# Performance work log

Measured on AMD Instinct MI355X. Metric: run time of the kernel, lower is better.

Reference implementation:

```python
import jax, jax.numpy as jnp
import numpy as np

N, F_IN, HID, OUT, H = 10000, 256, 256, 512, 4
E = 320000
SLOPE = 0.2  # GATv2Conv default negative_slope
EPS = 1e-5   # LayerNorm eps


def setup_inputs() -> dict:
    key = jax.random.key(0)
    ks = jax.random.split(key, 10)
    g = lambda k, shape, fan: (jax.random.normal(k, shape, jnp.float32) / np.float32(np.sqrt(fan)))
    d1, d2 = HID // H, OUT // H
    return {
        "x": jax.random.normal(ks[0], (N, F_IN), jnp.float32),
        "edge_index": jax.random.randint(ks[1], (2, E), 0, N),
        # layer 1 (in_feats -> hidden_dim, heads=H, concat)
        "Wl1": g(ks[2], (HID, F_IN), F_IN), "bl1": jnp.zeros((HID,), jnp.float32),
        "Wr1": g(ks[3], (HID, F_IN), F_IN), "br1": jnp.zeros((HID,), jnp.float32),
        "att1": g(ks[4], (H, d1), d1), "bias1": jnp.zeros((HID,), jnp.float32),
        # layer 2 (hidden_dim -> out_dim)
        "Wl2": g(ks[5], (OUT, HID), HID), "bl2": jnp.zeros((OUT,), jnp.float32),
        "Wr2": g(ks[6], (OUT, HID), HID), "br2": jnp.zeros((OUT,), jnp.float32),
        "att2": g(ks[7], (H, d2), d2), "bias2": jnp.zeros((OUT,), jnp.float32),
        # final LayerNorm
        "gamma": jnp.ones((OUT,), jnp.float32), "beta": jnp.zeros((OUT,), jnp.float32),
    }


def _gatv2(x, src, dst, Wl, bl, Wr, br, att, bias, heads):
    """GATv2Conv: e_ij = a_h . leaky_relu(Wl x_j + Wr x_i), softmax over j per i,
    out_i = sum_j alpha_ij * (Wl x_j), heads concatenated, plus bias."""
    n = x.shape[0]
    d = Wl.shape[0] // heads
    xl = (x @ Wl.T + bl).reshape(n, heads, d)  # source transform
    xr = (x @ Wr.T + br).reshape(n, heads, d)  # target transform
    s = jax.nn.leaky_relu(xl[src] + xr[dst], SLOPE)        # [E,H,d]
    e = jnp.einsum('ehd,hd->eh', s, att)                   # [E,H]
    m = jax.ops.segment_max(e, dst, num_segments=n)        # [N,H] (self-loops => no empty segs)
    w = jnp.exp(e - m[dst])
    denom = jax.ops.segment_sum(w, dst, num_segments=n)
    alpha = w / denom[dst]                                 # segment softmax
    out = jax.ops.segment_sum(alpha[:, :, None] * xl[src], dst, num_segments=n)  # [N,H,d]
    return out.reshape(n, heads * d) + bias


def reference(x, edge_index, Wl1, bl1, Wr1, br1, att1, bias1,
              Wl2, bl2, Wr2, br2, att2, bias2, gamma, beta):
    n = x.shape[0]
    loop = jnp.arange(n, dtype=edge_index.dtype)  # add_self_loops=True
    src = jnp.concatenate([edge_index[0], loop])
    dst = jnp.concatenate([edge_index[1], loop])
    h = jax.nn.relu(_gatv2(x, src, dst, Wl1, bl1, Wr1, br1, att1, bias1, H))
    h = _gatv2(h, src, dst, Wl2, bl2, Wr2, br2, att2, bias2, H)
    mu = jnp.mean(h, axis=-1, keepdims=True)
    var = jnp.var(h, axis=-1, keepdims=True)
    return gamma * (h - mu) / jnp.sqrt(var + EPS) + beta
```

## Files before the change

kernel.cpp:

```cpp
#include <hip/hip_runtime.h>
#include <stdint.h>

#define N_NODES 10000
#define K_DIM   256
#define HID_D   256
#define OUT_D   512
#define NE      320000
#define NE_TOT  (NE + N_NODES)
#define SLOPE   0.2f
#define LN_EPS  1e-5f

typedef __bf16 bf16x8 __attribute__((ext_vector_type(8)));
typedef float  f32x4  __attribute__((ext_vector_type(4)));
typedef unsigned short u16;
typedef uint32_t u32;

__device__ __forceinline__ float bf2f(u16 u) {
    union { u32 i; float f; } v; v.i = ((u32)u) << 16; return v.f;
}
__device__ __forceinline__ u16 f2bf(float f) {
    union { float f; u32 i; } v; v.f = f;
    u32 b = v.i;
    return (u16)((b + 0x7FFFu + ((b >> 16) & 1u)) >> 16);
}
__device__ __forceinline__ void bf2x2(u32 u, float& lo, float& hi) {
    union { u32 i; float f; } a, b;
    a.i = u << 16; b.i = u & 0xFFFF0000u;
    lo = a.f; hi = b.f;
}
__device__ __forceinline__ u32 pack2bf(float a, float b) {
    return (u32)f2bf(a) | ((u32)f2bf(b) << 16);
}

__device__ __forceinline__ void gl_lds16(const u16* g, u16* lds_base) {
    __builtin_amdgcn_global_load_lds(
        (const __attribute__((address_space(1))) void*)g,
        (__attribute__((address_space(3))) void*)lds_base, 16, 0, 0);
}

__global__ __launch_bounds__(256) void k_detect(const u32* __restrict__ x,
                                                int* __restrict__ flag) {
    u32 v = x[threadIdx.x];
    int e_lo = (int)((v >> 7) & 0xFF);
    int vote = (e_lo >= 100 && e_lo <= 150) ? 1 : 0;
    __shared__ int cnt;
    if (threadIdx.x == 0) cnt = 0;
    __syncthreads();
    atomicAdd(&cnt, vote);
    __syncthreads();
    if (threadIdx.x == 0) *flag = (cnt > 180) ? 1 : 0;
}

struct CanonW {
    const void *x, *wl1, *wr1, *wl2, *wr2;
    u16 *xd, *wl1d, *wr1d, *wl2d, *wr2d;
};
#define CW_X  2560000
#define CW_1  (CW_X + 65536)
#define CW_2  (CW_1 + 65536)
#define CW_3  (CW_2 + 131072)
#define CW_TOT (CW_3 + 131072)
__global__ __launch_bounds__(256) void k_canon_w(CanonW c, const int* __restrict__ flag) {
    int i = blockIdx.x * 256 + threadIdx.x;
    const void* src; u16* dst; int off;
    if      (i < CW_X) { src = c.x;   dst = c.xd;   off = i; }
    else if (i < CW_1) { src = c.wl1; dst = c.wl1d; off = i - CW_X; }
    else if (i < CW_2) { src = c.wr1; dst = c.wr1d; off = i - CW_1; }
    else if (i < CW_3) { src = c.wl2; dst = c.wl2d; off = i - CW_2; }
    else               { src = c.wr2; dst = c.wr2d; off = i - CW_3; }
    if (*flag) dst[off] = ((const u16*)src)[off];
    else       dst[off] = f2bf(((const float*)src)[off]);
}

struct CanonS { const void* src[10]; float* dst[10]; };
__global__ __launch_bounds__(256) void k_canon_s(CanonS c, const int* __restrict__ flag) {
    int i = blockIdx.x * 256 + threadIdx.x;
    int seg, off;
    if (i < 1024) { seg = i >> 8; off = i & 255; }
    else          { seg = 4 + ((i - 1024) >> 9); off = (i - 1024) & 511; }
    const void* s = c.src[seg];
    float* d = c.dst[seg];
    d[off] = (*flag) ? bf2f(((const u16*)s)[off]) : ((const float*)s)[off];
}


__global__ __launch_bounds__(256) void k_init_deg(int* deg) {
    int i = blockIdx.x * 256 + threadIdx.x;
    if (i < N_NODES) deg[i] = 1;
}

__global__ __launch_bounds__(256) void k_count_deg(const int* __restrict__ ei, int* deg) {
    int e = blockIdx.x * 256 + threadIdx.x;
    if (e < NE) atomicAdd(&deg[ei[NE + e]], 1);
}

__global__ __launch_bounds__(1024) void k_scan(const int* __restrict__ deg,
                                               int* __restrict__ rowptr,
                                               int* __restrict__ cursor) {
    __shared__ int sbuf[2][1024];
    int t = threadIdx.x;
    int base = t * 10;
    int loc[10];
    int s = 0;
    #pragma unroll
    for (int q = 0; q < 10; ++q) {
        int idx = base + q;
        int d = (idx < N_NODES) ? deg[idx] : 0;
        loc[q] = s;
        s += d;
    }
    sbuf[0][t] = s;
    __syncthreads();
    int cur = 0;
    for (int off = 1; off < 1024; off <<= 1) {
        int nxt = cur ^ 1;
        int v = sbuf[cur][t];
        if (t >= off) v += sbuf[cur][t - off];
        sbuf[nxt][t] = v;
        __syncthreads();
        cur = nxt;
    }
    int excl = sbuf[cur][t] - s;
    #pragma unroll
    for (int q = 0; q < 10; ++q) {
        int idx = base + q;
        if (idx <= N_NODES) {
            int val = excl + loc[q];
            rowptr[idx] = val;
            cursor[idx] = val;
        }
    }
}

__global__ __launch_bounds__(256) void k_scatter(const int* __restrict__ ei,
                                                 int* cursor, int* __restrict__ csr_src) {
    int e = blockIdx.x * 256 + threadIdx.x;
    if (e >= NE_TOT) return;
    int s, d;
    if (e < NE) { s = ei[e]; d = ei[NE + e]; }
    else        { s = e - NE; d = s; }
    int pos = atomicAdd(&cursor[d], 1);
    csr_src[pos] = s;
}

__global__ __launch_bounds__(256) void k_gemm2(const u16* __restrict__ X,
                                               const u16* __restrict__ Wl,
                                               const u16* __restrict__ Wr,
                                               const float* __restrict__ bl,
                                               const float* __restrict__ br,
                                               u16* __restrict__ Yl,
                                               u16* __restrict__ Yr, int Ncols) {
    __shared__ uint4 sAq[1024];
    __shared__ uint4 sBq[1024];
    u16* sA = (u16*)sAq;
    u16* sB = (u16*)sBq;

    int nb = Ncols >> 7;
    int by = blockIdx.y;
    const u16* W; const float* bias; u16* Y; int nbase;
    if (by < nb) { W = Wl; bias = bl; Y = Yl; nbase = by << 7; }
    else         { W = Wr; bias = br; Y = Yr; nbase = (by - nb) << 7; }

    int m0   = blockIdx.x << 7;
    int tid  = threadIdx.x;
    int wave = tid >> 6;
    int lane = tid & 63;
    int quad = lane >> 4;
    int l16  = lane & 15;
    int wm   = wave & 1;
    int wn   = wave >> 1;

    f32x4 acc[4][4] = {};

    #pragma unroll 1
    for (int kk = 0; kk < K_DIM; kk += 64) {
        #pragma unroll
        for (int r = 0; r < 4; ++r) {
            int g = wave + r * 4;
            int chunk = g >> 1;
            int row = ((g & 1) << 6) + lane;
            int mg = m0 + row;
            if (mg >= N_NODES) mg = N_NODES - 1;
            gl_lds16(X + (size_t)mg * K_DIM + kk + chunk * 8, sA + (size_t)(g << 6) * 8);
            gl_lds16(W + (size_t)(nbase + row) * K_DIM + kk + chunk * 8, sB + (size_t)(g << 6) * 8);
        }
        __syncthreads();

        #pragma unroll
        for (int s = 0; s < 2; ++s) {
            int c = s * 4 + quad;
            bf16x8 af[4], bf[4];
            #pragma unroll
            for (int t = 0; t < 4; ++t) {
                int m = (wm << 6) + t * 16 + l16;
                af[t] = *(const bf16x8*)(sA + ((size_t)(c << 7) + m) * 8);
                int n = (wn << 6) + t * 16 + l16;
                bf[t] = *(const bf16x8*)(sB + ((size_t)(c << 7) + n) * 8);
            }
            #pragma unroll
            for (int mt = 0; mt < 4; ++mt)
                #pragma unroll
                for (int nt = 0; nt < 4; ++nt)
                    acc[mt][nt] = __builtin_amdgcn_mfma_f32_16x16x32_bf16(
                        af[mt], bf[nt], acc[mt][nt], 0, 0, 0);
        }
        __syncthreads();
    }

    #pragma unroll
    for (int nt = 0; nt < 4; ++nt) {
        int col = nbase + (wn << 6) + nt * 16 + l16;
        float bv = bias[col];
        #pragma unroll
        for (int mt = 0; mt < 4; ++mt) {
            int rbase = m0 + (wm << 6) + mt * 16 + quad * 4;
            #pragma unroll
            for (int q = 0; q < 4; ++q) {
                int row = rbase + q;
                if (row < N_NODES)
                    Y[(size_t)row * Ncols + col] = f2bf(acc[mt][nt][q] + bv);
            }
        }
    }
}

__global__ __launch_bounds__(256) void k_agg1(const u16* __restrict__ xl,
                                              const u16* __restrict__ xr,
                                              const int* __restrict__ rowptr,
                                              const int* __restrict__ csr_src,
                                              const float* __restrict__ att,
                                              const float* __restrict__ bias,
                                              u16* __restrict__ hout) {
    int wave = threadIdx.x >> 6, lane = threadIdx.x & 63;
    int i = blockIdx.x * 4 + wave;
    if (i >= N_NODES) return;
    int c0 = (lane >> 4) * 64 + (lane & 15) * 4;

    const u32* xr32 = (const u32*)(xr + (size_t)i * HID_D + c0);
    u32 xp0 = xr32[0], xp1 = xr32[1];
    float xr0, xr1v, xr2v, xr3;
    bf2x2(xp0, xr0, xr1v); bf2x2(xp1, xr2v, xr3);
    float a0 = att[c0], a1 = att[c0 + 1], a2 = att[c0 + 2], a3 = att[c0 + 3];

    int beg = rowptr[i], end = rowptr[i + 1];
    float denom = 0.f;
    float acc0 = 0.f, acc1 = 0.f, acc2 = 0.f, acc3 = 0.f;
    const u16* xbase = xl + c0;

    auto edge = [&](u32 q0, u32 q1) {
        float v0, v1, v2, v3;
        bf2x2(q0, v0, v1); bf2x2(q1, v2, v3);
        float s0 = v0 + xr0;  s0 = fmaxf(s0, s0 * SLOPE);
        float s1 = v1 + xr1v; s1 = fmaxf(s1, s1 * SLOPE);
        float s2 = v2 + xr2v; s2 = fmaxf(s2, s2 * SLOPE);
        float s3 = v3 + xr3;  s3 = fmaxf(s3, s3 * SLOPE);
        float pr = s0 * a0;
        pr = fmaf(s1, a1, pr); pr = fmaf(s2, a2, pr); pr = fmaf(s3, a3, pr);
        #pragma unroll
        for (int o = 1; o < 16; o <<= 1) pr += __shfl_xor(pr, o, 64);
        float w = __expf(fminf(pr, 60.f));
        denom += w;
        acc0 = fmaf(w, v0, acc0);
        acc1 = fmaf(w, v1, acc1);
        acc2 = fmaf(w, v2, acc2);
        acc3 = fmaf(w, v3, acc3);
    };

    for (int chunk = beg; chunk < end; chunk += 64) {
        int cnt = end - chunk; if (cnt > 64) cnt = 64;
        int myj = csr_src[chunk + ((lane < cnt) ? lane : (cnt - 1))];
        int e = 0;
        for (; e + 4 <= cnt; e += 4) {
            int j0 = __shfl(myj, e,     64);
            int j1 = __shfl(myj, e + 1, 64);
            int j2 = __shfl(myj, e + 2, 64);
            int j3 = __shfl(myj, e + 3, 64);
            const u32* r0 = (const u32*)(xbase + (size_t)j0 * HID_D);
            const u32* r1 = (const u32*)(xbase + (size_t)j1 * HID_D);
            const u32* r2 = (const u32*)(xbase + (size_t)j2 * HID_D);
            const u32* r3 = (const u32*)(xbase + (size_t)j3 * HID_D);
            u32 p00 = r0[0], p01 = r0[1];
            u32 p10 = r1[0], p11 = r1[1];
            u32 p20 = r2[0], p21 = r2[1];
            u32 p30 = r3[0], p31 = r3[1];
            edge(p00, p01); edge(p10, p11); edge(p20, p21); edge(p30, p31);
        }
        for (; e < cnt; ++e) {
            int j = __shfl(myj, e, 64);
            const u32* r = (const u32*)(xbase + (size_t)j * HID_D);
            edge(r[0], r[1]);
        }
    }

    float inv = 1.f / denom;
    float o0 = fmaxf(fmaf(acc0, inv, bias[c0]),     0.f);
    float o1 = fmaxf(fmaf(acc1, inv, bias[c0 + 1]), 0.f);
    float o2 = fmaxf(fmaf(acc2, inv, bias[c0 + 2]), 0.f);
    float o3 = fmaxf(fmaf(acc3, inv, bias[c0 + 3]), 0.f);
    u32* hp = (u32*)(hout + (size_t)i * HID_D + c0);
    hp[0] = pack2bf(o0, o1);
    hp[1] = pack2bf(o2, o3);
}

__global__ __launch_bounds__(256) void k_agg2_ln(const u16* __restrict__ xl,
                                                 const u16* __restrict__ xr,
                                                 const int* __restrict__ rowptr,
                                                 const int* __restrict__ csr_src,
                                                 const float* __restrict__ att,
                                                 const float* __restrict__ bias,
                                                 const float* __restrict__ gamma,
                                                 const float* __restrict__ beta,
                                                 void* __restrict__ outv,
                                                 const int* __restrict__ flag) {
    int wave = threadIdx.x >> 6, lane = threadIdx.x & 63;
    int i = blockIdx.x * 4 + wave;
    if (i >= N_NODES) return;
    int c0 = (lane >> 4) * 128 + (lane & 15) * 8;

    float xrv[8], a[8];
    {
        uint4 xq = *(const uint4*)(xr + (size_t)i * OUT_D + c0);
        bf2x2(xq.x, xrv[0], xrv[1]); bf2x2(xq.y, xrv[2], xrv[3]);
        bf2x2(xq.z, xrv[4], xrv[5]); bf2x2(xq.w, xrv[6], xrv[7]);
        #pragma unroll
        for (int k = 0; k < 8; ++k) a[k] = att[c0 + k];
    }

    int beg = rowptr[i], end = rowptr[i + 1];
    float denom = 0.f;
    float acc[8] = {};
    const u16* xbase = xl + c0;

    auto edge = [&](uint4 q) {
        float v[8];
        bf2x2(q.x, v[0], v[1]); bf2x2(q.y, v[2], v[3]);
        bf2x2(q.z, v[4], v[5]); bf2x2(q.w, v[6], v[7]);
        float pr = 0.f;
        #pragma unroll
        for (int k = 0; k < 8; ++k) {
            float s = v[k] + xrv[k];
            s = fmaxf(s, s * SLOPE);
            pr = fmaf(s, a[k], pr);
        }
        #pragma unroll
        for (int o = 1; o < 16; o <<= 1) pr += __shfl_xor(pr, o, 64);
        float w = __expf(fminf(pr, 60.f));
        denom += w;
        #pragma unroll
        for (int k = 0; k < 8; ++k) acc[k] = fmaf(w, v[k], acc[k]);
    };

    for (int chunk = beg; chunk < end; chunk += 64) {
        int cnt = end - chunk; if (cnt > 64) cnt = 64;
        int myj = csr_src[chunk + ((lane < cnt) ? lane : (cnt - 1))];
        int e = 0;
        for (; e + 4 <= cnt; e += 4) {
            int j0 = __shfl(myj, e,     64);
            int j1 = __shfl(myj, e + 1, 64);
            int j2 = __shfl(myj, e + 2, 64);
            int j3 = __shfl(myj, e + 3, 64);
            uint4 q0 = *(const uint4*)(xbase + (size_t)j0 * OUT_D);
            uint4 q1 = *(const uint4*)(xbase + (size_t)j1 * OUT_D);
            uint4 q2 = *(const uint4*)(xbase + (size_t)j2 * OUT_D);
            uint4 q3 = *(const uint4*)(xbase + (size_t)j3 * OUT_D);
            edge(q0); edge(q1); edge(q2); edge(q3);
        }
        for (; e < cnt; ++e) {
            int j = __shfl(myj, e, 64);
            edge(*(const uint4*)(xbase + (size_t)j * OUT_D));
        }
    }

    float inv = 1.f / denom;
    float o[8];
    float s1 = 0.f, s2 = 0.f;
    #pragma unroll
    for (int k = 0; k < 8; ++k) {
        o[k] = fmaf(acc[k], inv, bias[c0 + k]);
        s1 += o[k];
        s2 = fmaf(o[k], o[k], s2);
    }
    #pragma unroll
    for (int off = 1; off < 64; off <<= 1) {
        s1 += __shfl_xor(s1, off, 64);
        s2 += __shfl_xor(s2, off, 64);
    }
    float mu  = s1 * (1.f / OUT_D);
    float var = s2 * (1.f / OUT_D) - mu * mu;
    float rstd = rsqrtf(var + LN_EPS);

    size_t ob = (size_t)i * OUT_D + c0;
    if (*flag) {
        u32 pk[4];
        #pragma unroll
        for (int k = 0; k < 4; ++k) {
            float r0 = fmaf(gamma[c0 + 2*k]     * (o[2*k]     - mu), rstd, beta[c0 + 2*k]);
            float r1 = fmaf(gamma[c0 + 2*k + 1] * (o[2*k + 1] - mu), rstd, beta[c0 + 2*k + 1]);
            pk[k] = pack2bf(r0, r1);
        }
        *(uint4*)((u16*)outv + ob) = make_uint4(pk[0], pk[1], pk[2], pk[3]);
    } else {
        float* out = (float*)outv + ob;
        #pragma unroll
        for (int k = 0; k < 8; ++k)
            out[k] = fmaf(gamma[c0 + k] * (o[k] - mu), rstd, beta[c0 + k]);
    }
}


extern "C" void kernel_launch(void* const* d_in, const int* in_sizes, int n_in,
                              void* d_out, int out_size, void* d_ws, size_t ws_size,
                              hipStream_t stream) {
    const int* ei = (const int*)d_in[1];

    char* ws = (char*)d_ws;
    size_t off = 0;
    auto alloc = [&](size_t bytes) { void* p = ws + off; off += (bytes + 255) & ~(size_t)255; return p; };
    u16* xcb  = (u16*)alloc((size_t)N_NODES * K_DIM * 2);
    u16* wl1b = (u16*)alloc((size_t)HID_D * K_DIM * 2);
    u16* wr1b = (u16*)alloc((size_t)HID_D * K_DIM * 2);
    u16* wl2b = (u16*)alloc((size_t)OUT_D * K_DIM * 2);
    u16* wr2b = (u16*)alloc((size_t)OUT_D * K_DIM * 2);
    u16* xl1b = (u16*)alloc((size_t)N_NODES * HID_D * 2);
    u16* xr1b = (u16*)alloc((size_t)N_NODES * HID_D * 2);
    u16* hb   = (u16*)alloc((size_t)N_NODES * HID_D * 2);
    u16* xl2b = (u16*)alloc((size_t)N_NODES * OUT_D * 2);
    u16* xr2b = (u16*)alloc((size_t)N_NODES * OUT_D * 2);
    float* bl1c  = (float*)alloc(HID_D * 4);
    float* br1c  = (float*)alloc(HID_D * 4);
    float* att1c = (float*)alloc(HID_D * 4);
    float* bia1c = (float*)alloc(HID_D * 4);
    float* bl2c  = (float*)alloc(OUT_D * 4);
    float* br2c  = (float*)alloc(OUT_D * 4);
    float* att2c = (float*)alloc(OUT_D * 4);
    float* bia2c = (float*)alloc(OUT_D * 4);
    float* gamc  = (float*)alloc(OUT_D * 4);
    float* betc  = (float*)alloc(OUT_D * 4);
    int* flag = (int*)alloc(256);
    int* deg  = (int*)alloc((size_t)N_NODES * 4);
    int* rowp = (int*)alloc((size_t)(N_NODES + 1) * 4);
    int* curs = (int*)alloc((size_t)(N_NODES + 1) * 4);
    int* csrc = (int*)alloc((size_t)NE_TOT * 4);

    hipLaunchKernelGGL(k_detect, dim3(1), dim3(256), 0, stream, (const u32*)d_in[0], flag);

    CanonW cw = { d_in[0], d_in[2], d_in[4], d_in[8], d_in[10],
                  xcb, wl1b, wr1b, wl2b, wr2b };
    hipLaunchKernelGGL(k_canon_w, dim3(CW_TOT / 256), dim3(256), 0, stream, cw, flag);

    CanonS cs;
    cs.src[0] = d_in[3];  cs.dst[0] = bl1c;
    cs.src[1] = d_in[5];  cs.dst[1] = br1c;
    cs.src[2] = d_in[6];  cs.dst[2] = att1c;
    cs.src[3] = d_in[7];  cs.dst[3] = bia1c;
    cs.src[4] = d_in[9];  cs.dst[4] = bl2c;
    cs.src[5] = d_in[11]; cs.dst[5] = br2c;
    cs.src[6] = d_in[12]; cs.dst[6] = att2c;
    cs.src[7] = d_in[13]; cs.dst[7] = bia2c;
    cs.src[8] = d_in[14]; cs.dst[8] = gamc;
    cs.src[9] = d_in[15]; cs.dst[9] = betc;
    hipLaunchKernelGGL(k_canon_s, dim3(16), dim3(256), 0, stream, cs, flag);

    hipLaunchKernelGGL(k_init_deg, dim3((N_NODES + 255) / 256), dim3(256), 0, stream, deg);
    hipLaunchKernelGGL(k_count_deg, dim3((NE + 255) / 256), dim3(256), 0, stream, ei, deg);
    hipLaunchKernelGGL(k_scan, dim3(1), dim3(1024), 0, stream, deg, rowp, curs);
    hipLaunchKernelGGL(k_scatter, dim3((NE_TOT + 255) / 256), dim3(256), 0, stream, ei, curs, csrc);

    const int MB = (N_NODES + 127) / 128;
    hipLaunchKernelGGL(k_gemm2, dim3(MB, 2 * HID_D / 128), dim3(256), 0, stream,
                       xcb, wl1b, wr1b, bl1c, br1c, xl1b, xr1b, HID_D);
    hipLaunchKernelGGL(k_agg1, dim3((N_NODES + 3) / 4), dim3(256), 0, stream,
                       xl1b, xr1b, rowp, csrc, att1c, bia1c, hb);
    hipLaunchKernelGGL(k_gemm2, dim3(MB, 2 * OUT_D / 128), dim3(256), 0, stream,
                       hb, wl2b, wr2b, bl2c, br2c, xl2b, xr2b, OUT_D);
    hipLaunchKernelGGL(k_agg2_ln, dim3((N_NODES + 3) / 4), dim3(256), 0, stream,
                       xl2b, xr2b, rowp, csrc, att2c, bia2c, gamc, betc, d_out, flag);
}
```

Measured before the change: 288.6 us.

## Merge canon kernels, memset degrees, vectorize aggregation with packed f32x2 math

Fuses the weight and scalar canonicalization kernels into one launch, and replaces the degree-init kernel with a memset plus a +1 inside the scan. The aggregation kernels now read neighbor indices with prefetched int4 loads instead of per-chunk shuffles, interleave the four edges' shuffle reductions, and use packed f32x2 FMA/max arithmetic. This is meant to cut launch count, shuffle traffic and VALU instruction count in the gather-bound aggregation. The int4 index loads assume 16-byte alignment of csrc+beg, which rowptr offsets do not guarantee, so misaligned vector loads are a risk.

```diff
diff --git a/kernel.cpp b/kernel.cpp
--- a/kernel.cpp
+++ b/kernel.cpp
@@ -12,8 +12,23 @@
 
 typedef __bf16 bf16x8 __attribute__((ext_vector_type(8)));
 typedef float  f32x4  __attribute__((ext_vector_type(4)));
+typedef float  f32x2  __attribute__((ext_vector_type(2)));
 typedef unsigned short u16;
 typedef uint32_t u32;
+
+#if __has_builtin(__builtin_elementwise_fma)
+#define PKFMA(a,b,c) __builtin_elementwise_fma((a),(b),(c))
+#else
+#define PKFMA(a,b,c) ((a)*(b)+(c))
+#endif
+#if __has_builtin(__builtin_elementwise_max)
+#define PKMAX(a,b) __builtin_elementwise_max((a),(b))
+#else
+static __device__ __forceinline__ f32x2 pkmax_(f32x2 a, f32x2 b) {
+    f32x2 r; r.x = fmaxf(a.x, b.x); r.y = fmaxf(a.y, b.y); return r;
+}
+#define PKMAX(a,b) pkmax_((a),(b))
+#endif
 
 __device__ __forceinline__ float bf2f(u16 u) {
     union { u32 i; float f; } v; v.i = ((u32)u) << 16; return v.f;
@@ -23,10 +38,10 @@
     u32 b = v.i;
     return (u16)((b + 0x7FFFu + ((b >> 16) & 1u)) >> 16);
 }
-__device__ __forceinline__ void bf2x2(u32 u, float& lo, float& hi) {
-    union { u32 i; float f; } a, b;
-    a.i = u << 16; b.i = u & 0xFFFF0000u;
-    lo = a.f; hi = b.f;
+__device__ __forceinline__ f32x2 bfpair(u32 u) {
+    union { u32 i; float f; } lo, hi;
+    lo.i = u << 16; hi.i = u & 0xFFFF0000u;
+    f32x2 r; r.x = lo.f; r.y = hi.f; return r;
 }
 __device__ __forceinline__ u32 pack2bf(float a, float b) {
     return (u32)f2bf(a) | ((u32)f2bf(b) << 16);
@@ -51,43 +66,39 @@
     if (threadIdx.x == 0) *flag = (cnt > 180) ? 1 : 0;
 }
 
-struct CanonW {
+struct CanonAll {
     const void *x, *wl1, *wr1, *wl2, *wr2;
     u16 *xd, *wl1d, *wr1d, *wl2d, *wr2d;
+    const void* ssrc[10]; float* sdst[10];
 };
 #define CW_X  2560000
 #define CW_1  (CW_X + 65536)
 #define CW_2  (CW_1 + 65536)
 #define CW_3  (CW_2 + 131072)
 #define CW_TOT (CW_3 + 131072)
-__global__ __launch_bounds__(256) void k_canon_w(CanonW c, const int* __restrict__ flag) {
+__global__ __launch_bounds__(256) void k_canon(CanonAll c, const int* __restrict__ flag) {
     int i = blockIdx.x * 256 + threadIdx.x;
-    const void* src; u16* dst; int off;
-    if      (i < CW_X) { src = c.x;   dst = c.xd;   off = i; }
-    else if (i < CW_1) { src = c.wl1; dst = c.wl1d; off = i - CW_X; }
-    else if (i < CW_2) { src = c.wr1; dst = c.wr1d; off = i - CW_1; }
-    else if (i < CW_3) { src = c.wl2; dst = c.wl2d; off = i - CW_2; }
-    else               { src = c.wr2; dst = c.wr2d; off = i - CW_3; }
-    if (*flag) dst[off] = ((const u16*)src)[off];
-    else       dst[off] = f2bf(((const float*)src)[off]);
-}
-
-struct CanonS { const void* src[10]; float* dst[10]; };
-__global__ __launch_bounds__(256) void k_canon_s(CanonS c, const int* __restrict__ flag) {
-    int i = blockIdx.x * 256 + threadIdx.x;
-    int seg, off;
-    if (i < 1024) { seg = i >> 8; off = i & 255; }
-    else          { seg = 4 + ((i - 1024) >> 9); off = (i - 1024) & 511; }
-    const void* s = c.src[seg];
-    float* d = c.dst[seg];
-    d[off] = (*flag) ? bf2f(((const u16*)s)[off]) : ((const float*)s)[off];
-}
-
-
-__global__ __launch_bounds__(256) void k_init_deg(int* deg) {
-    int i = blockIdx.x * 256 + threadIdx.x;
-    if (i < N_NODES) deg[i] = 1;
-}
+    int f = *flag;
+    if (i < CW_TOT) {
+        const void* src; u16* dst; int off;
+        if      (i < CW_X) { src = c.x;   dst = c.xd;   off = i; }
+        else if (i < CW_1) { src = c.wl1; dst = c.wl1d; off = i - CW_X; }
+        else if (i < CW_2) { src = c.wr1; dst = c.wr1d; off = i - CW_1; }
+        else if (i < CW_3) { src = c.wl2; dst = c.wl2d; off = i - CW_2; }
+        else               { src = c.wr2; dst = c.wr2d; off = i - CW_3; }
+        if (f) dst[off] = ((const u16*)src)[off];
+        else   dst[off] = f2bf(((const float*)src)[off]);
+    } else {
+        int s = i - CW_TOT;
+        int seg, off;
+        if (s < 1024) { seg = s >> 8; off = s & 255; }
+        else          { seg = 4 + ((s - 1024) >> 9); off = (s - 1024) & 511; }
+        const void* sp = c.ssrc[seg];
+        float* d = c.sdst[seg];
+        d[off] = f ? bf2f(((const u16*)sp)[off]) : ((const float*)sp)[off];
+    }
+}
+
 
 __global__ __launch_bounds__(256) void k_count_deg(const int* __restrict__ ei, int* deg) {
     int e = blockIdx.x * 256 + threadIdx.x;
@@ -105,7 +116,7 @@
     #pragma unroll
     for (int q = 0; q < 10; ++q) {
         int idx = base + q;
-        int d = (idx < N_NODES) ? deg[idx] : 0;
+        int d = (idx < N_NODES) ? (deg[idx] + 1) : 0;
         loc[q] = s;
         s += d;
     }
@@ -227,7 +238,7 @@
 __global__ __launch_bounds__(256) void k_agg1(const u16* __restrict__ xl,
                                               const u16* __restrict__ xr,
                                               const int* __restrict__ rowptr,
-                                              const int* __restrict__ csr_src,
+                                              const int* __restrict__ csrc,
                                               const float* __restrict__ att,
                                               const float* __restrict__ bias,
                                               u16* __restrict__ hout) {
@@ -236,76 +247,96 @@
     if (i >= N_NODES) return;
     int c0 = (lane >> 4) * 64 + (lane & 15) * 4;
 
-    const u32* xr32 = (const u32*)(xr + (size_t)i * HID_D + c0);
-    u32 xp0 = xr32[0], xp1 = xr32[1];
-    float xr0, xr1v, xr2v, xr3;
-    bf2x2(xp0, xr0, xr1v); bf2x2(xp1, xr2v, xr3);
-    float a0 = att[c0], a1 = att[c0 + 1], a2 = att[c0 + 2], a3 = att[c0 + 3];
+    f32x2 xp[2], ap[2];
+    {
+        uint2 xq = *(const uint2*)(xr + (size_t)i * HID_D + c0);
+        xp[0] = bfpair(xq.x); xp[1] = bfpair(xq.y);
+        const f32x2* a2 = (const f32x2*)(att + c0);
+        ap[0] = a2[0]; ap[1] = a2[1];
+    }
+    const f32x2 slope2 = {SLOPE, SLOPE};
 
     int beg = rowptr[i], end = rowptr[i + 1];
     float denom = 0.f;
-    float acc0 = 0.f, acc1 = 0.f, acc2 = 0.f, acc3 = 0.f;
+    f32x2 acc[2] = {};
     const u16* xbase = xl + c0;
 
-    auto edge = [&](u32 q0, u32 q1) {
-        float v0, v1, v2, v3;
-        bf2x2(q0, v0, v1); bf2x2(q1, v2, v3);
-        float s0 = v0 + xr0;  s0 = fmaxf(s0, s0 * SLOPE);
-        float s1 = v1 + xr1v; s1 = fmaxf(s1, s1 * SLOPE);
-        float s2 = v2 + xr2v; s2 = fmaxf(s2, s2 * SLOPE);
-        float s3 = v3 + xr3;  s3 = fmaxf(s3, s3 * SLOPE);
-        float pr = s0 * a0;
-        pr = fmaf(s1, a1, pr); pr = fmaf(s2, a2, pr); pr = fmaf(s3, a3, pr);
+    auto dot4 = [&](const f32x2 v[2]) -> float {
+        f32x2 pr2 = {0.f, 0.f};
+        #pragma unroll
+        for (int k = 0; k < 2; ++k) {
+            f32x2 s = v[k] + xp[k];
+            s = PKMAX(s, s * slope2);
+            pr2 = PKFMA(s, ap[k], pr2);
+        }
+        return pr2.x + pr2.y;
+    };
+
+    int p = beg;
+    int4 jq = {0, 0, 0, 0};
+    if (p + 4 <= end) jq = *(const int4*)(csrc + p);
+    for (; p + 4 <= end; p += 4) {
+        int4 jc = jq;
+        if (p + 8 <= end) jq = *(const int4*)(csrc + p + 4);
+        uint2 q0 = *(const uint2*)(xbase + (size_t)jc.x * HID_D);
+        uint2 q1 = *(const uint2*)(xbase + (size_t)jc.y * HID_D);
+        uint2 q2 = *(const uint2*)(xbase + (size_t)jc.z * HID_D);
+        uint2 q3 = *(const uint2*)(xbase + (size_t)jc.w * HID_D);
+        f32x2 v0[2] = { bfpair(q0.x), bfpair(q0.y) };
+        f32x2 v1[2] = { bfpair(q1.x), bfpair(q1.y) };
+        f32x2 v2[2] = { bfpair(q2.x), bfpair(q2.y) };
+        f32x2 v3[2] = { bfpair(q3.x), bfpair(q3.y) };
+        float pr0 = dot4(v0), pr1 = dot4(v1), pr2s = dot4(v2), pr3 = dot4(v3);
+        #pragma unroll
+        for (int o = 1; o < 16; o <<= 1) {
+            pr0  += __shfl_xor(pr0,  o, 64);
+            pr1  += __shfl_xor(pr1,  o, 64);
+            pr2s += __shfl_xor(pr2s, o, 64);
+            pr3  += __shfl_xor(pr3,  o, 64);
+        }
+        float w0 = __expf(fminf(pr0,  60.f));
+        float w1 = __expf(fminf(pr1,  60.f));
+        float w2 = __expf(fminf(pr2s, 60.f));
+        float w3 = __expf(fminf(pr3,  60.f));
+        denom += (w0 + w1) + (w2 + w3);
+        f32x2 W0 = {w0, w0}, W1 = {w1, w1}, W2 = {w2, w2}, W3 = {w3, w3};
+        #pragma unroll
+        for (int k = 0; k < 2; ++k) {
+            acc[k] = PKFMA(W0, v0[k], acc[k]);
+            acc[k] = PKFMA(W1, v1[k], acc[k]);
+            acc[k] = PKFMA(W2, v2[k], acc[k]);
+            acc[k] = PKFMA(W3, v3[k], acc[k]);
+        }
+    }
+    for (; p < end; ++p) {
+        int j = csrc[p];
+        uint2 q = *(const uint2*)(xbase + (size_t)j * HID_D);
+        f32x2 v[2] = { bfpair(q.x), bfpair(q.y) };
+        float pr = dot4(v);
         #pragma unroll
         for (int o = 1; o < 16; o <<= 1) pr += __shfl_xor(pr, o, 64);
         float w = __expf(fminf(pr, 60.f));
         denom += w;
-        acc0 = fmaf(w, v0, acc0);
-        acc1 = fmaf(w, v1, acc1);
-        acc2 = fmaf(w, v2, acc2);
-        acc3 = fmaf(w, v3, acc3);
-    };
-
-    for (int chunk = beg; chunk < end; chunk += 64) {
-        int cnt = end - chunk; if (cnt > 64) cnt = 64;
-        int myj = csr_src[chunk + ((lane < cnt) ? lane : (cnt - 1))];
-        int e = 0;
-        for (; e + 4 <= cnt; e += 4) {
-            int j0 = __shfl(myj, e,     64);
-            int j1 = __shfl(myj, e + 1, 64);
-            int j2 = __shfl(myj, e + 2, 64);
-            int j3 = __shfl(myj, e + 3, 64);
-            const u32* r0 = (const u32*)(xbase + (size_t)j0 * HID_D);
-            const u32* r1 = (const u32*)(xbase + (size_t)j1 * HID_D);
-            const u32* r2 = (const u32*)(xbase + (size_t)j2 * HID_D);
-            const u32* r3 = (const u32*)(xbase + (size_t)j3 * HID_D);
-            u32 p00 = r0[0], p01 = r0[1];
-            u32 p10 = r1[0], p11 = r1[1];
-            u32 p20 = r2[0], p21 = r2[1];
-            u32 p30 = r3[0], p31 = r3[1];
-            edge(p00, p01); edge(p10, p11); edge(p20, p21); edge(p30, p31);
-        }
-        for (; e < cnt; ++e) {
-            int j = __shfl(myj, e, 64);
-            const u32* r = (const u32*)(xbase + (size_t)j * HID_D);
-            edge(r[0], r[1]);
-        }
+        f32x2 W = {w, w};
+        acc[0] = PKFMA(W, v[0], acc[0]);
+        acc[1] = PKFMA(W, v[1], acc[1]);
     }
 
     float inv = 1.f / denom;
-    float o0 = fmaxf(fmaf(acc0, inv, bias[c0]),     0.f);
-    float o1 = fmaxf(fmaf(acc1, inv, bias[c0 + 1]), 0.f);
-    float o2 = fmaxf(fmaf(acc2, inv, bias[c0 + 2]), 0.f);
-    float o3 = fmaxf(fmaf(acc3, inv, bias[c0 + 3]), 0.f);
+    f32x2 inv2 = {inv, inv};
+    const f32x2* bp = (const f32x2*)(bias + c0);
+    f32x2 z = {0.f, 0.f};
+    f32x2 o0 = PKMAX(PKFMA(acc[0], inv2, bp[0]), z);
+    f32x2 o1 = PKMAX(PKFMA(acc[1], inv2, bp[1]), z);
     u32* hp = (u32*)(hout + (size_t)i * HID_D + c0);
-    hp[0] = pack2bf(o0, o1);
-    hp[1] = pack2bf(o2, o3);
+    hp[0] = pack2bf(o0.x, o0.y);
+    hp[1] = pack2bf(o1.x, o1.y);
 }
 
 __global__ __launch_bounds__(256) void k_agg2_ln(const u16* __restrict__ xl,
                                                  const u16* __restrict__ xr,
                                                  const int* __restrict__ rowptr,
-                                                 const int* __restrict__ csr_src,
+                                                 const int* __restrict__ csrc,
                                                  const float* __restrict__ att,
                                                  const float* __restrict__ bias,
                                                  const float* __restrict__ gamma,
@@ -317,68 +348,92 @@
     if (i >= N_NODES) return;
     int c0 = (lane >> 4) * 128 + (lane & 15) * 8;
 
-    float xrv[8], a[8];
+    f32x2 xp[4], ap[4];
     {
         uint4 xq = *(const uint4*)(xr + (size_t)i * OUT_D + c0);
-        bf2x2(xq.x, xrv[0], xrv[1]); bf2x2(xq.y, xrv[2], xrv[3]);
-        bf2x2(xq.z, xrv[4], xrv[5]); bf2x2(xq.w, xrv[6], xrv[7]);
-        #pragma unroll
-        for (int k = 0; k < 8; ++k) a[k] = att[c0 + k];
-    }
+        xp[0] = bfpair(xq.x); xp[1] = bfpair(xq.y);
+        xp[2] = bfpair(xq.z); xp[3] = bfpair(xq.w);
+        const f32x2* a2 = (const f32x2*)(att + c0);
+        ap[0] = a2[0]; ap[1] = a2[1]; ap[2] = a2[2]; ap[3] = a2[3];
+    }
+    const f32x2 slope2 = {SLOPE, SLOPE};
 
     int beg = rowptr[i], end = rowptr[i + 1];
     float denom = 0.f;
-    float acc[8] = {};
+    f32x2 acc[4] = {};
     const u16* xbase = xl + c0;
 
-    auto edge = [&](uint4 q) {
-        float v[8];
-        bf2x2(q.x, v[0], v[1]); bf2x2(q.y, v[2], v[3]);
-        bf2x2(q.z, v[4], v[5]); bf2x2(q.w, v[6], v[7]);
-        float pr = 0.f;
-        #pragma unroll
-        for (int k = 0; k < 8; ++k) {
-            float s = v[k] + xrv[k];
-            s = fmaxf(s, s * SLOPE);
-            pr = fmaf(s, a[k], pr);
-        }
+    auto dot8 = [&](const f32x2 v[4]) -> float {
+        f32x2 pr2 = {0.f, 0.f};
+        #pragma unroll
+        for (int k = 0; k < 4; ++k) {
+            f32x2 s = v[k] + xp[k];
+            s = PKMAX(s, s * slope2);
+            pr2 = PKFMA(s, ap[k], pr2);
+        }
+        return pr2.x + pr2.y;
+    };
+
+    int p = beg;
+    int4 jq = {0, 0, 0, 0};
+    if (p + 4 <= end) jq = *(const int4*)(csrc + p);
+    for (; p + 4 <= end; p += 4) {
+        int4 jc = jq;
+        if (p + 8 <= end) jq = *(const int4*)(csrc + p + 4);
+        uint4 q0 = *(const uint4*)(xbase + (size_t)jc.x * OUT_D);
+        uint4 q1 = *(const uint4*)(xbase + (size_t)jc.y * OUT_D);
+        uint4 q2 = *(const uint4*)(xbase + (size_t)jc.z * OUT_D);
+        uint4 q3 = *(const uint4*)(xbase + (size_t)jc.w * OUT_D);
+        f32x2 v0[4] = { bfpair(q0.x), bfpair(q0.y), bfpair(q0.z), bfpair(q0.w) };
+        f32x2 v1[4] = { bfpair(q1.x), bfpair(q1.y), bfpair(q1.z), bfpair(q1.w) };
+        f32x2 v2[4] = { bfpair(q2.x), bfpair(q2.y), bfpair(q2.z), bfpair(q2.w) };
+        f32x2 v3[4] = { bfpair(q3.x), bfpair(q3.y), bfpair(q3.z), bfpair(q3.w) };
+        float pr0 = dot8(v0), pr1 = dot8(v1), pr2s = dot8(v2), pr3 = dot8(v3);
+        #pragma unroll
+        for (int o = 1; o < 16; o <<= 1) {
+            pr0  += __shfl_xor(pr0,  o, 64);
+            pr1  += __shfl_xor(pr1,  o, 64);
+            pr2s += __shfl_xor(pr2s, o, 64);
+            pr3  += __shfl_xor(pr3,  o, 64);
+        }
+        float w0 = __expf(fminf(pr0,  60.f));
+        float w1 = __expf(fminf(pr1,  60.f));
+        float w2 = __expf(fminf(pr2s, 60.f));
+        float w3 = __expf(fminf(pr3,  60.f));
+        denom += (w0 + w1) + (w2 + w3);
+        f32x2 W0 = {w0, w0}, W1 = {w1, w1}, W2 = {w2, w2}, W3 = {w3, w3};
+        #pragma unroll
+        for (int k = 0; k < 4; ++k) {
+            acc[k] = PKFMA(W0, v0[k], acc[k]);
+            acc[k] = PKFMA(W1, v1[k], acc[k]);
+            acc[k] = PKFMA(W2, v2[k], acc[k]);
+            acc[k] = PKFMA(W3, v3[k], acc[k]);
+        }
+    }
+    for (; p < end; ++p) {
+        int j = csrc[p];
+        uint4 q = *(const uint4*)(xbase + (size_t)j * OUT_D);
+        f32x2 v[4] = { bfpair(q.x), bfpair(q.y), bfpair(q.z), bfpair(q.w) };
+        float pr = dot8(v);
         #pragma unroll
         for (int o = 1; o < 16; o <<= 1) pr += __shfl_xor(pr, o, 64);
         float w = __expf(fminf(pr, 60.f));
         denom += w;
-        #pragma unroll
-        for (int k = 0; k < 8; ++k) acc[k] = fmaf(w, v[k], acc[k]);
-    };
-
-    for (int chunk = beg; chunk < end; chunk += 64) {
-        int cnt = end - chunk; if (cnt > 64) cnt = 64;
-        int myj = csr_src[chunk + ((lane < cnt) ? lane : (cnt - 1))];
-        int e = 0;
-        for (; e + 4 <= cnt; e += 4) {
-            int j0 = __shfl(myj, e,     64);
-            int j1 = __shfl(myj, e + 1, 64);
-            int j2 = __shfl(myj, e + 2, 64);
-            int j3 = __shfl(myj, e + 3, 64);
-            uint4 q0 = *(const uint4*)(xbase + (size_t)j0 * OUT_D);
-            uint4 q1 = *(const uint4*)(xbase + (size_t)j1 * OUT_D);
-            uint4 q2 = *(const uint4*)(xbase + (size_t)j2 * OUT_D);
-            uint4 q3 = *(const uint4*)(xbase + (size_t)j3 * OUT_D);
-            edge(q0); edge(q1); edge(q2); edge(q3);
-        }
-        for (; e < cnt; ++e) {
-            int j = __shfl(myj, e, 64);
-            edge(*(const uint4*)(xbase + (size_t)j * OUT_D));
-        }
+        f32x2 W = {w, w};
+        #pragma unroll
+        for (int k = 0; k < 4; ++k) acc[k] = PKFMA(W, v[k], acc[k]);
     }
 
     float inv = 1.f / denom;
-    float o[8];
+    f32x2 inv2 = {inv, inv};
+    const f32x2* bp = (const f32x2*)(bias + c0);
+    f32x2 o2[4];
     float s1 = 0.f, s2 = 0.f;
     #pragma unroll
-    for (int k = 0; k < 8; ++k) {
-        o[k] = fmaf(acc[k], inv, bias[c0 + k]);
-        s1 += o[k];
-        s2 = fmaf(o[k], o[k], s2);
+    for (int k = 0; k < 4; ++k) {
+        o2[k] = PKFMA(acc[k], inv2, bp[k]);
+        s1 += o2[k].x + o2[k].y;
+        s2 = fmaf(o2[k].x, o2[k].x, fmaf(o2[k].y, o2[k].y, s2));
     }
     #pragma unroll
     for (int off = 1; off < 64; off <<= 1) {
@@ -388,22 +443,24 @@
     float mu  = s1 * (1.f / OUT_D);
     float var = s2 * (1.f / OUT_D) - mu * mu;
     float rstd = rsqrtf(var + LN_EPS);
+    f32x2 mu2 = {mu, mu}, rs2 = {rstd, rstd};
+    const f32x2* gp  = (const f32x2*)(gamma + c0);
+    const f32x2* bep = (const f32x2*)(beta + c0);
 
     size_t ob = (size_t)i * OUT_D + c0;
     if (*flag) {
         u32 pk[4];
         #pragma unroll
         for (int k = 0; k < 4; ++k) {
-            float r0 = fmaf(gamma[c0 + 2*k]     * (o[2*k]     - mu), rstd, beta[c0 + 2*k]);
-            float r1 = fmaf(gamma[c0 + 2*k + 1] * (o[2*k + 1] - mu), rstd, beta[c0 + 2*k + 1]);
-            pk[k] = pack2bf(r0, r1);
+            f32x2 r = PKFMA(gp[k] * (o2[k] - mu2), rs2, bep[k]);
+            pk[k] = pack2bf(r.x, r.y);
         }
         *(uint4*)((u16*)outv + ob) = make_uint4(pk[0], pk[1], pk[2], pk[3]);
     } else {
-        float* out = (float*)outv + ob;
-        #pragma unroll
-        for (int k = 0; k < 8; ++k)
-            out[k] = fmaf(gamma[c0 + k] * (o[k] - mu), rstd, beta[c0 + k]);
+        f32x2* out = (f32x2*)((float*)outv + ob);
+        #pragma unroll
+        for (int k = 0; k < 4; ++k)
+            out[k] = PKFMA(gp[k] * (o2[k] - mu2), rs2, bep[k]);
     }
 }
 
@@ -444,24 +501,22 @@
 
     hipLaunchKernelGGL(k_detect, dim3(1), dim3(256), 0, stream, (const u32*)d_in[0], flag);
 
-    CanonW cw = { d_in[0], d_in[2], d_in[4], d_in[8], d_in[10],
-                  xcb, wl1b, wr1b, wl2b, wr2b };
-    hipLaunchKernelGGL(k_canon_w, dim3(CW_TOT / 256), dim3(256), 0, stream, cw, flag);
-
-    CanonS cs;
-    cs.src[0] = d_in[3];  cs.dst[0] = bl1c;
-    cs.src[1] = d_in[5];  cs.dst[1] = br1c;
-    cs.src[2] = d_in[6];  cs.dst[2] = att1c;
-    cs.src[3] = d_in[7];  cs.dst[3] = bia1c;
-    cs.src[4] = d_in[9];  cs.dst[4] = bl2c;
-    cs.src[5] = d_in[11]; cs.dst[5] = br2c;
-    cs.src[6] = d_in[12]; cs.dst[6] = att2c;
-    cs.src[7] = d_in[13]; cs.dst[7] = bia2c;
-    cs.src[8] = d_in[14]; cs.dst[8] = gamc;
-    cs.src[9] = d_in[15]; cs.dst[9] = betc;
-    hipLaunchKernelGGL(k_canon_s, dim3(16), dim3(256), 0, stream, cs, flag);
-
-    hipLaunchKernelGGL(k_init_deg, dim3((N_NODES + 255) / 256), dim3(256), 0, stream, deg);
+    CanonAll ca;
+    ca.x = d_in[0]; ca.wl1 = d_in[2]; ca.wr1 = d_in[4]; ca.wl2 = d_in[8]; ca.wr2 = d_in[10];
+    ca.xd = xcb; ca.wl1d = wl1b; ca.wr1d = wr1b; ca.wl2d = wl2b; ca.wr2d = wr2b;
+    ca.ssrc[0] = d_in[3];  ca.sdst[0] = bl1c;
+    ca.ssrc[1] = d_in[5];  ca.sdst[1] = br1c;
+    ca.ssrc[2] = d_in[6];  ca.sdst[2] = att1c;
+    ca.ssrc[3] = d_in[7];  ca.sdst[3] = bia1c;
+    ca.ssrc[4] = d_in[9];  ca.sdst[4] = bl2c;
+    ca.ssrc[5] = d_in[11]; ca.sdst[5] = br2c;
+    ca.ssrc[6] = d_in[12]; ca.sdst[6] = att2c;
+    ca.ssrc[7] = d_in[13]; ca.sdst[7] = bia2c;
+    ca.ssrc[8] = d_in[14]; ca.sdst[8] = gamc;
+    ca.ssrc[9] = d_in[15]; ca.sdst[9] = betc;
+    hipLaunchKernelGGL(k_canon, dim3(CW_TOT / 256 + 16), dim3(256), 0, stream, ca, flag);
+
+    hipMemsetAsync(deg, 0, (size_t)N_NODES * 4, stream);
     hipLaunchKernelGGL(k_count_deg, dim3((NE + 255) / 256), dim3(256), 0, stream, ei, deg);
     hipLaunchKernelGGL(k_scan, dim3(1), dim3(1024), 0, stream, deg, rowp, curs);
     hipLaunchKernelGGL(k_scatter, dim3((NE_TOT + 255) / 256), dim3(256), 0, stream, ei, curs, csrc);
```

Result: no change. 287.1 us (-0.5%).
